# Kernel optimization log

Hardware: AMD Instinct MI355X
Metric: run time of the kernel (lower is better)

Reference implementation:

```python
import jax, jax.numpy as jnp
import numpy as np

D_IN = 1024
D_OUT = 1024
NUM_HEADS = 16
HEAD_DIM = D_OUT // NUM_HEADS


def setup_inputs() -> dict:
    key = jax.random.key(0)
    ks = jax.random.split(key, 6)
    s = 1.0 / np.sqrt(D_IN)
    x = jax.random.normal(ks[0], (2, 2048, D_IN), dtype=jnp.float32)
    Wq = jax.random.uniform(ks[1], (D_IN, D_OUT), jnp.float32, -s, s)
    Wk = jax.random.uniform(ks[2], (D_IN, D_OUT), jnp.float32, -s, s)
    Wv = jax.random.uniform(ks[3], (D_IN, D_OUT), jnp.float32, -s, s)
    Wo = jax.random.uniform(ks[4], (D_OUT, D_OUT), jnp.float32, -s, s)
    bo = jax.random.uniform(ks[5], (D_OUT,), jnp.float32, -s, s)
    return {"x": x, "Wq": Wq, "Wk": Wk, "Wv": Wv, "Wo": Wo, "bo": bo}


def reference(x, Wq, Wk, Wv, Wo, bo):
    b, s, _ = x.shape
    # Note: source assigns keys = W_query(x), queries = W_key(x) (swapped names);
    # replicate exactly.
    keys = (x @ Wq).reshape(b, s, NUM_HEADS, HEAD_DIM)
    values = (x @ Wv).reshape(b, s, NUM_HEADS, HEAD_DIM)
    queries = (x @ Wk).reshape(b, s, NUM_HEADS, HEAD_DIM)
    # [b, h, q, k] attention scores; source's masked_fill is non in-place and
    # discarded, so NO causal mask is applied (faithful to the bug).
    scores = jnp.einsum("bqhd,bkhd->bhqk", queries, keys)
    attn = jax.nn.softmax(scores / np.sqrt(HEAD_DIM), axis=-1)
    # dropout p=0.0 -> identity
    ctx = jnp.einsum("bhqk,bkhd->bqhd", attn, values).reshape(b, s, D_OUT)
    return ctx @ Wo + bo
```

## Files before the change

kernel.cpp:

```cpp
#include <hip/hip_runtime.h>
#include <math.h>

#define DI 1024
#define SQ 2048
#define NB 2
#define NH 16
#define HD 64
#define QSCALE 0.18033688f

typedef __attribute__((ext_vector_type(8))) short short8;
typedef __attribute__((ext_vector_type(4))) float f32x4;
typedef __attribute__((ext_vector_type(16))) float f32x16;
typedef __attribute__((ext_vector_type(2))) unsigned int uint2v;
typedef __attribute__((ext_vector_type(4))) int int4v;
typedef __attribute__((ext_vector_type(4))) unsigned short ushort4v;

static __device__ __forceinline__ unsigned short f2bf(float f) {
    union { float f; unsigned u; } v; v.f = f;
    unsigned r = v.u + 0x7FFFu + ((v.u >> 16) & 1u);
    return (unsigned short)(r >> 16);
}
static __device__ __forceinline__ float fexp2(float x) {
    float r; asm("v_exp_f32 %0, %1" : "=v"(r) : "v"(x)); return r;
}
static __device__ __forceinline__ unsigned cvtpk(float lo, float hi) {
    unsigned r; asm("v_cvt_pk_bf16_f32 %0, %1, %2" : "=v"(r) : "v"(lo), "v"(hi)); return r;
}
static __device__ __forceinline__ void plswap(unsigned& a, unsigned& b) {
    asm volatile("v_permlane32_swap_b32 %0, %1" : "+v"(a), "+v"(b));
}
static __device__ __forceinline__ short8 pack4(unsigned a, unsigned b, unsigned c, unsigned d) {
    union { unsigned u[4]; short8 s; } x; x.u[0] = a; x.u[1] = b; x.u[2] = c; x.u[3] = d; return x.s;
}

typedef __attribute__((address_space(1))) const unsigned int gas_uint;
typedef __attribute__((address_space(3))) unsigned int las_uint;
static __device__ __forceinline__ void gload16(const void* g, void* l) {
    __builtin_amdgcn_global_load_lds((gas_uint*)g, (las_uint*)l, 16, 0, 0);
}
#define RAW_BARRIER() __builtin_amdgcn_s_barrier()
#define WAIT_VM4()  do { asm volatile("s_waitcnt vmcnt(4)" ::: "memory"); \
                         __builtin_amdgcn_sched_barrier(0); } while (0)
#define WAIT_VM0()  do { asm volatile("s_waitcnt vmcnt(0)" ::: "memory"); \
                         __builtin_amdgcn_sched_barrier(0); } while (0)

#define MFMA16(a, b, c) __builtin_amdgcn_mfma_f32_16x16x32_bf16(a, b, c, 0, 0, 0)
#define MFMA32(a, b, c) __builtin_amdgcn_mfma_f32_32x32x16_bf16(a, b, c, 0, 0, 0)

__global__ __launch_bounds__(256) void k_cvt_bf16(const float* __restrict__ src,
                                                  unsigned short* __restrict__ dst) {
    int i = blockIdx.x * 256 + threadIdx.x;
    const f32x4* s4 = (const f32x4*)src + (size_t)i * 2;
    f32x4 a = s4[0], b = s4[1];
    ushort4v o0, o1;
    o0[0] = f2bf(a[0]); o0[1] = f2bf(a[1]); o0[2] = f2bf(a[2]); o0[3] = f2bf(a[3]);
    o1[0] = f2bf(b[0]); o1[1] = f2bf(b[1]); o1[2] = f2bf(b[2]); o1[3] = f2bf(b[3]);
    *(ushort4v*)(dst + (size_t)i * 8)     = o0;
    *(ushort4v*)(dst + (size_t)i * 8 + 4) = o1;
}

__global__ __launch_bounds__(256) void k_transpose_w4(const float* __restrict__ W0, const float* __restrict__ W1,
                                                      const float* __restrict__ W2, const float* __restrict__ W3,
                                                      unsigned short* __restrict__ T0, unsigned short* __restrict__ T1,
                                                      unsigned short* __restrict__ T2, unsigned short* __restrict__ T3) {
    const float* W; unsigned short* T;
    switch (blockIdx.z) {
        case 0: W = W0; T = T0; break;
        case 1: W = W1; T = T1; break;
        case 2: W = W2; T = T2; break;
        default: W = W3; T = T3; break;
    }
    __shared__ float t[32][33];
    int tx = threadIdx.x, ty = threadIdx.y;
    int n0 = blockIdx.x * 32, k0 = blockIdx.y * 32;
#pragma unroll
    for (int j = 0; j < 32; j += 8) t[ty + j][tx] = W[(size_t)(k0 + ty + j) * DI + n0 + tx];
    __syncthreads();
#pragma unroll
    for (int j = 0; j < 32; j += 8)
        T[(size_t)(n0 + ty + j) * DI + k0 + tx] = f2bf(t[tx][ty + j]);
}

template <int MODE>
__global__ __launch_bounds__(256) void k_gemm(const unsigned short* __restrict__ A,
                                              const unsigned short* __restrict__ Bt,
                                              unsigned short* __restrict__ oK,
                                              unsigned short* __restrict__ oQ,
                                              unsigned short* __restrict__ oV,
                                              const float* __restrict__ bias) {
    __shared__ __align__(16) unsigned short As[2][128 * 32];
    __shared__ __align__(16) unsigned short Bs[2][128 * 32];
    const int tid = threadIdx.x, lane = tid & 63, w = tid >> 6;
    const int wr = w >> 1, wc = w & 1;
    const int tm = blockIdx.y, tn = blockIdx.x;
    const unsigned short* Abase = A  + (size_t)tm * 128 * DI;
    const unsigned short* Bbase = Bt + (size_t)tn * 128 * DI;

    auto stage = [&](int kt, int bi) {
#pragma unroll
        for (int i = 0; i < 2; ++i) {
            int u = tid + i * 256;
            int row = u >> 2, c8 = (u & 3) * 8;
            gload16(Abase + (size_t)row * DI + kt * 32 + c8, &As[bi][u * 8]);
            gload16(Bbase + (size_t)row * DI + kt * 32 + c8, &Bs[bi][u * 8]);
        }
    };

    f32x4 acc[4][4] = {};
    stage(0, 0);
    for (int kt = 0; kt < DI / 32; ++kt) {
        RAW_BARRIER();
        if (kt + 1 < DI / 32) { stage(kt + 1, (kt + 1) & 1); WAIT_VM4(); }
        else                  { WAIT_VM0(); }
        const int bi = kt & 1;
        short8 af[4], bf[4];
#pragma unroll
        for (int mi = 0; mi < 4; ++mi)
            af[mi] = *(const short8*)&As[bi][(wr * 64 + mi * 16 + (lane & 15)) * 32 + (lane >> 4) * 8];
#pragma unroll
        for (int ni = 0; ni < 4; ++ni)
            bf[ni] = *(const short8*)&Bs[bi][(wc * 64 + ni * 16 + (lane & 15)) * 32 + (lane >> 4) * 8];
        __builtin_amdgcn_s_setprio(1);
#pragma unroll
        for (int mi = 0; mi < 4; ++mi)
#pragma unroll
            for (int ni = 0; ni < 4; ++ni)
                acc[mi][ni] = MFMA16(af[mi], bf[ni], acc[mi][ni]);
        __builtin_amdgcn_s_setprio(0);
    }

    if (MODE == 2) {
        float bv[4];
#pragma unroll
        for (int ni = 0; ni < 4; ++ni) bv[ni] = bias[tn * 128 + wc * 64 + ni * 16 + (lane & 15)];
        float* Co = (float*)oK;
#pragma unroll
        for (int mi = 0; mi < 4; ++mi)
#pragma unroll
            for (int ni = 0; ni < 4; ++ni)
#pragma unroll
                for (int j = 0; j < 4; ++j) {
                    int m = tm * 128 + wr * 64 + mi * 16 + (lane >> 4) * 4 + j;
                    int n = tn * 128 + wc * 64 + ni * 16 + (lane & 15);
                    Co[(size_t)m * DI + n] = acc[mi][ni][j] + bv[ni];
                }
    } else {
        const int which = tn >> 3;
        if (which < 2) {
            unsigned short* Co = which ? oQ : oK;
            const float scl = which ? QSCALE : 1.0f;
#pragma unroll
            for (int mi = 0; mi < 4; ++mi)
#pragma unroll
                for (int ni = 0; ni < 4; ++ni)
#pragma unroll
                    for (int j = 0; j < 4; ++j) {
                        int m = tm * 128 + wr * 64 + mi * 16 + (lane >> 4) * 4 + j;
                        int n = (tn & 7) * 128 + wc * 64 + ni * 16 + (lane & 15);
                        Co[(((size_t)(m >> 11) * NH + (n >> 6)) * SQ + (m & 2047)) * HD + (n & 63)] =
                            f2bf(acc[mi][ni][j] * scl);
                    }
        } else {
#pragma unroll
            for (int mi = 0; mi < 4; ++mi)
#pragma unroll
                for (int ni = 0; ni < 4; ++ni) {
                    uint2v pk;
                    pk[0] = cvtpk(acc[mi][ni][0], acc[mi][ni][1]);
                    pk[1] = cvtpk(acc[mi][ni][2], acc[mi][ni][3]);
                    int m = tm * 128 + wr * 64 + mi * 16 + (lane >> 4) * 4;
                    int n = (tn & 7) * 128 + wc * 64 + ni * 16 + (lane & 15);
                    *(uint2v*)&oV[(((size_t)(m >> 11) * NH + (n >> 6)) * HD + (n & 63)) * SQ + (m & 2047)] = pk;
                }
        }
    }
}

__global__ __launch_bounds__(256) void k_attn(const unsigned short* __restrict__ Q,
                                              const unsigned short* __restrict__ K,
                                              const unsigned short* __restrict__ Vt,
                                              unsigned short* __restrict__ ctx) {
    __shared__ __align__(16) unsigned short smem[16384];
    unsigned short* Ks = smem;
    unsigned short* Vs = smem + 8192;
    const int tid = threadIdx.x, lane = tid & 63, w = tid >> 6;
    const int hi = lane >> 5, l31 = lane & 31;

    const int wg = (blockIdx.x & 7) * 64 + (blockIdx.x >> 3);
    const int bh = wg >> 4;
    const int q0 = (wg & 15) * 128;

    const unsigned short* qh = Q  + (size_t)bh * SQ * HD;
    const unsigned short* kh = K  + (size_t)bh * SQ * HD;
    const unsigned short* vh = Vt + (size_t)bh * HD * SQ;

    short8 qf[4];
#pragma unroll
    for (int ks = 0; ks < 4; ++ks)
        qf[ks] = *(const short8*)(qh + (size_t)(q0 + w * 32 + l31) * HD + ks * 16 + hi * 8);

    short8 ones;
#pragma unroll
    for (int i = 0; i < 8; ++i) ones[i] = (short)0x3F80;

    f32x16 o[2] = {{0}, {0}};
    f32x16 od = {};

    auto stage = [&](int kt, int bi) {
#pragma unroll
        for (int i = 0; i < 2; ++i) {
            int u = tid + i * 256;
            int row = u >> 3, c = u & 7;
            int cs = c ^ (row & 7);
            gload16(kh + (size_t)(kt * 64 + row) * HD + cs * 8, Ks + bi * 4096 + u * 8);
            gload16(vh + (size_t)row * SQ + kt * 64 + cs * 8, Vs + bi * 4096 + u * 8);
        }
    };

    stage(0, 0);
    for (int kt = 0; kt < SQ / 64; ++kt) {
        RAW_BARRIER();
        if (kt + 1 < SQ / 64) { stage(kt + 1, (kt + 1) & 1); WAIT_VM4(); }
        else                  { WAIT_VM0(); }
        const unsigned short* kb_ = Ks + (kt & 1) * 4096;
        const unsigned short* vb_ = Vs + (kt & 1) * 4096;

#pragma unroll
        for (int kb = 0; kb < 2; ++kb) {
            f32x16 s = {};
            {
                short8 kf[4];
#pragma unroll
                for (int ks = 0; ks < 4; ++ks) {
                    int row = kb * 32 + l31;
                    kf[ks] = *(const short8*)&kb_[row * 64 + (((ks * 2 + hi) ^ (row & 7)) * 8)];
                }
                __builtin_amdgcn_s_setprio(1);
#pragma unroll
                for (int ks = 0; ks < 4; ++ks) s = MFMA32(kf[ks], qf[ks], s);
                __builtin_amdgcn_s_setprio(0);
            }

            float p[16];
#pragma unroll
            for (int r = 0; r < 16; ++r) p[r] = fexp2(s[r]);

            unsigned g0 = cvtpk(p[0],  p[1]),  g1 = cvtpk(p[2],  p[3]);
            unsigned g2 = cvtpk(p[4],  p[5]),  g3 = cvtpk(p[6],  p[7]);
            unsigned g4 = cvtpk(p[8],  p[9]),  g5 = cvtpk(p[10], p[11]);
            unsigned g6 = cvtpk(p[12], p[13]), g7 = cvtpk(p[14], p[15]);
            plswap(g0, g2); plswap(g1, g3);
            plswap(g4, g6); plswap(g5, g7);
            short8 pf[2] = { pack4(g0, g1, g2, g3), pack4(g4, g5, g6, g7) };

            short8 vf[2][2];
#pragma unroll
            for (int ks2 = 0; ks2 < 2; ++ks2)
#pragma unroll
                for (int da = 0; da < 2; ++da) {
                    int row = da * 32 + l31;
                    vf[ks2][da] = *(const short8*)&vb_[row * 64 + (((kb * 4 + ks2 * 2 + hi) ^ (row & 7)) * 8)];
                }
            __builtin_amdgcn_s_setprio(1);
#pragma unroll
            for (int ks2 = 0; ks2 < 2; ++ks2) {
#pragma unroll
                for (int da = 0; da < 2; ++da)
                    o[da] = MFMA32(vf[ks2][da], pf[ks2], o[da]);
                od = MFMA32(ones, pf[ks2], od);
            }
            __builtin_amdgcn_s_setprio(0);
        }
    }

    __syncthreads();

    float inv = 1.0f / od[0];

    unsigned short* osc = smem + w * 2304;
#pragma unroll
    for (int da = 0; da < 2; ++da)
#pragma unroll
        for (int g = 0; g < 4; ++g) {
            uint2v pk;
            pk[0] = cvtpk(o[da][4 * g]     * inv, o[da][4 * g + 1] * inv);
            pk[1] = cvtpk(o[da][4 * g + 2] * inv, o[da][4 * g + 3] * inv);
            int d = da * 32 + 8 * g + 4 * hi;
            *(uint2v*)&osc[l31 * 72 + d] = pk;
        }
    __syncthreads();

    const int b = bh >> 4, h = bh & 15;
#pragma unroll
    for (int rr = 0; rr < 4; ++rr) {
        int qrow = rr * 8 + (lane >> 3), ck = lane & 7;
        int4v vv = *(const int4v*)&osc[qrow * 72 + ck * 8];
        *(int4v*)&ctx[((size_t)(b * SQ + q0 + w * 32 + qrow)) * DI + h * 64 + ck * 8] = vv;
    }
}

extern "C" void kernel_launch(void* const* d_in, const int* in_sizes, int n_in,
                              void* d_out, int out_size, void* d_ws, size_t ws_size,
                              hipStream_t stream) {
    const float* x  = (const float*)d_in[0];
    const float* Wq = (const float*)d_in[1];
    const float* Wk = (const float*)d_in[2];
    const float* Wv = (const float*)d_in[3];
    const float* Wo = (const float*)d_in[4];
    const float* bo = (const float*)d_in[5];

    char* ws = (char*)d_ws;
    unsigned short* xb   = (unsigned short*)(ws);
    unsigned short* Wall = (unsigned short*)(ws + (8u  << 20));
    unsigned short* Wot  = (unsigned short*)(ws + (14u << 20));
    unsigned short* Qh   = (unsigned short*)(ws + (16u << 20));
    unsigned short* Kh   = (unsigned short*)(ws + (24u << 20));
    unsigned short* Vt   = (unsigned short*)(ws + (32u << 20));
    unsigned short* ctx  = (unsigned short*)(ws + (40u << 20));

    k_cvt_bf16<<<2048, 256, 0, stream>>>(x, xb);
    k_transpose_w4<<<dim3(32, 32, 4), dim3(32, 8), 0, stream>>>(
        Wq, Wk, Wv, Wo, Wall, Wall + (1u << 20), Wall + (2u << 20), Wot);

    k_gemm<0><<<dim3(24, 32), 256, 0, stream>>>(xb, Wall, Kh, Qh, Vt, nullptr);

    k_attn<<<dim3(512), 256, 0, stream>>>(Qh, Kh, Vt, ctx);

    k_gemm<2><<<dim3(8, 32), 256, 0, stream>>>(ctx, Wot, (unsigned short*)d_out, nullptr, nullptr, bo);
}
```

Measured before the change: 121.4 us.

## Triple-buffer LDS tiles and restructure attention loop for more MFMA overlap

Moves both the projection GEMM and the attention kernel from double to triple buffering in LDS. The next tile is issued and waited on before the barrier, so one barrier per iteration suffices. In the attention kernel, all K/V fragments for both 32-key sub-blocks are loaded up front, both score MFMAs run back to back, and two separate output accumulators are used and summed at the end. The goal is fewer stalls from MFMA dependency chains and from barriers, at the cost of more LDS and more registers, which may reduce occupancy.

```diff
diff --git a/kernel.cpp b/kernel.cpp
--- a/kernel.cpp
+++ b/kernel.cpp
@@ -38,7 +38,8 @@
 static __device__ __forceinline__ void gload16(const void* g, void* l) {
     __builtin_amdgcn_global_load_lds((gas_uint*)g, (las_uint*)l, 16, 0, 0);
 }
-#define RAW_BARRIER() __builtin_amdgcn_s_barrier()
+#define RAW_BARRIER() do { __builtin_amdgcn_s_barrier(); \
+                           __builtin_amdgcn_sched_barrier(0); } while (0)
 #define WAIT_VM4()  do { asm volatile("s_waitcnt vmcnt(4)" ::: "memory"); \
                          __builtin_amdgcn_sched_barrier(0); } while (0)
 #define WAIT_VM0()  do { asm volatile("s_waitcnt vmcnt(0)" ::: "memory"); \
@@ -88,8 +89,8 @@
                                               unsigned short* __restrict__ oQ,
                                               unsigned short* __restrict__ oV,
                                               const float* __restrict__ bias) {
-    __shared__ __align__(16) unsigned short As[2][128 * 32];
-    __shared__ __align__(16) unsigned short Bs[2][128 * 32];
+    __shared__ __align__(16) unsigned short As[3][128 * 32];
+    __shared__ __align__(16) unsigned short Bs[3][128 * 32];
     const int tid = threadIdx.x, lane = tid & 63, w = tid >> 6;
     const int wr = w >> 1, wc = w & 1;
     const int tm = blockIdx.y, tn = blockIdx.x;
@@ -109,10 +110,10 @@
     f32x4 acc[4][4] = {};
     stage(0, 0);
     for (int kt = 0; kt < DI / 32; ++kt) {
+        if (kt + 1 < DI / 32) { stage(kt + 1, (kt + 1) % 3); WAIT_VM4(); }
+        else                  { WAIT_VM0(); }
         RAW_BARRIER();
-        if (kt + 1 < DI / 32) { stage(kt + 1, (kt + 1) & 1); WAIT_VM4(); }
-        else                  { WAIT_VM0(); }
-        const int bi = kt & 1;
+        const int bi = kt % 3;
         short8 af[4], bf[4];
 #pragma unroll
         for (int mi = 0; mi < 4; ++mi)
@@ -180,9 +181,9 @@
                                               const unsigned short* __restrict__ K,
                                               const unsigned short* __restrict__ Vt,
                                               unsigned short* __restrict__ ctx) {
-    __shared__ __align__(16) unsigned short smem[16384];
+    __shared__ __align__(16) unsigned short smem[24576];
     unsigned short* Ks = smem;
-    unsigned short* Vs = smem + 8192;
+    unsigned short* Vs = smem + 12288;
     const int tid = threadIdx.x, lane = tid & 63, w = tid >> 6;
     const int hi = lane >> 5, l31 = lane & 31;
 
@@ -203,7 +204,8 @@
 #pragma unroll
     for (int i = 0; i < 8; ++i) ones[i] = (short)0x3F80;
 
-    f32x16 o[2] = {{0}, {0}};
+    f32x16 oA[2] = {{0}, {0}};
+    f32x16 oB[2] = {{0}, {0}};
     f32x16 od = {};
 
     auto stage = [&](int kt, int bi) {
@@ -219,58 +221,74 @@
 
     stage(0, 0);
     for (int kt = 0; kt < SQ / 64; ++kt) {
+        if (kt + 1 < SQ / 64) { stage(kt + 1, (kt + 1) % 3); WAIT_VM4(); }
+        else                  { WAIT_VM0(); }
         RAW_BARRIER();
-        if (kt + 1 < SQ / 64) { stage(kt + 1, (kt + 1) & 1); WAIT_VM4(); }
-        else                  { WAIT_VM0(); }
-        const unsigned short* kb_ = Ks + (kt & 1) * 4096;
-        const unsigned short* vb_ = Vs + (kt & 1) * 4096;
-
-#pragma unroll
-        for (int kb = 0; kb < 2; ++kb) {
-            f32x16 s = {};
-            {
-                short8 kf[4];
-#pragma unroll
-                for (int ks = 0; ks < 4; ++ks) {
-                    int row = kb * 32 + l31;
-                    kf[ks] = *(const short8*)&kb_[row * 64 + (((ks * 2 + hi) ^ (row & 7)) * 8)];
-                }
-                __builtin_amdgcn_s_setprio(1);
-#pragma unroll
-                for (int ks = 0; ks < 4; ++ks) s = MFMA32(kf[ks], qf[ks], s);
-                __builtin_amdgcn_s_setprio(0);
+        const unsigned short* kb_ = Ks + (kt % 3) * 4096;
+        const unsigned short* vb_ = Vs + (kt % 3) * 4096;
+
+        short8 kf[2][4], vf[2][2][2];
+#pragma unroll
+        for (int kb = 0; kb < 2; ++kb)
+#pragma unroll
+            for (int ks = 0; ks < 4; ++ks) {
+                int row = kb * 32 + l31;
+                kf[kb][ks] = *(const short8*)&kb_[row * 64 + (((ks * 2 + hi) ^ (row & 7)) * 8)];
             }
-
-            float p[16];
-#pragma unroll
-            for (int r = 0; r < 16; ++r) p[r] = fexp2(s[r]);
-
-            unsigned g0 = cvtpk(p[0],  p[1]),  g1 = cvtpk(p[2],  p[3]);
-            unsigned g2 = cvtpk(p[4],  p[5]),  g3 = cvtpk(p[6],  p[7]);
-            unsigned g4 = cvtpk(p[8],  p[9]),  g5 = cvtpk(p[10], p[11]);
-            unsigned g6 = cvtpk(p[12], p[13]), g7 = cvtpk(p[14], p[15]);
-            plswap(g0, g2); plswap(g1, g3);
-            plswap(g4, g6); plswap(g5, g7);
-            short8 pf[2] = { pack4(g0, g1, g2, g3), pack4(g4, g5, g6, g7) };
-
-            short8 vf[2][2];
+#pragma unroll
+        for (int kb = 0; kb < 2; ++kb)
 #pragma unroll
             for (int ks2 = 0; ks2 < 2; ++ks2)
 #pragma unroll
                 for (int da = 0; da < 2; ++da) {
                     int row = da * 32 + l31;
-                    vf[ks2][da] = *(const short8*)&vb_[row * 64 + (((kb * 4 + ks2 * 2 + hi) ^ (row & 7)) * 8)];
+                    vf[kb][ks2][da] = *(const short8*)&vb_[row * 64 + (((kb * 4 + ks2 * 2 + hi) ^ (row & 7)) * 8)];
                 }
-            __builtin_amdgcn_s_setprio(1);
-#pragma unroll
-            for (int ks2 = 0; ks2 < 2; ++ks2) {
-#pragma unroll
-                for (int da = 0; da < 2; ++da)
-                    o[da] = MFMA32(vf[ks2][da], pf[ks2], o[da]);
-                od = MFMA32(ones, pf[ks2], od);
-            }
-            __builtin_amdgcn_s_setprio(0);
-        }
+
+        f32x16 s0 = {}, s1 = {};
+        __builtin_amdgcn_s_setprio(1);
+#pragma unroll
+        for (int ks = 0; ks < 4; ++ks) s0 = MFMA32(kf[0][ks], qf[ks], s0);
+#pragma unroll
+        for (int ks = 0; ks < 4; ++ks) s1 = MFMA32(kf[1][ks], qf[ks], s1);
+        __builtin_amdgcn_s_setprio(0);
+
+        float p0[16], p1[16];
+#pragma unroll
+        for (int r = 0; r < 16; ++r) p0[r] = fexp2(s0[r]);
+#pragma unroll
+        for (int r = 0; r < 16; ++r) p1[r] = fexp2(s1[r]);
+
+        unsigned a0 = cvtpk(p0[0],  p0[1]),  a1 = cvtpk(p0[2],  p0[3]);
+        unsigned a2 = cvtpk(p0[4],  p0[5]),  a3 = cvtpk(p0[6],  p0[7]);
+        unsigned a4 = cvtpk(p0[8],  p0[9]),  a5 = cvtpk(p0[10], p0[11]);
+        unsigned a6 = cvtpk(p0[12], p0[13]), a7 = cvtpk(p0[14], p0[15]);
+        plswap(a0, a2); plswap(a1, a3); plswap(a4, a6); plswap(a5, a7);
+        short8 pf0[2] = { pack4(a0, a1, a2, a3), pack4(a4, a5, a6, a7) };
+
+        unsigned b0 = cvtpk(p1[0],  p1[1]),  b1 = cvtpk(p1[2],  p1[3]);
+        unsigned b2 = cvtpk(p1[4],  p1[5]),  b3 = cvtpk(p1[6],  p1[7]);
+        unsigned b4 = cvtpk(p1[8],  p1[9]),  b5 = cvtpk(p1[10], p1[11]);
+        unsigned b6 = cvtpk(p1[12], p1[13]), b7 = cvtpk(p1[14], p1[15]);
+        plswap(b0, b2); plswap(b1, b3); plswap(b4, b6); plswap(b5, b7);
+        short8 pf1[2] = { pack4(b0, b1, b2, b3), pack4(b4, b5, b6, b7) };
+
+        __builtin_amdgcn_s_setprio(1);
+#pragma unroll
+        for (int ks2 = 0; ks2 < 2; ++ks2) {
+#pragma unroll
+            for (int da = 0; da < 2; ++da)
+                oA[da] = MFMA32(vf[0][ks2][da], pf0[ks2], oA[da]);
+            od = MFMA32(ones, pf0[ks2], od);
+        }
+#pragma unroll
+        for (int ks2 = 0; ks2 < 2; ++ks2) {
+#pragma unroll
+            for (int da = 0; da < 2; ++da)
+                oB[da] = MFMA32(vf[1][ks2][da], pf1[ks2], oB[da]);
+            od = MFMA32(ones, pf1[ks2], od);
+        }
+        __builtin_amdgcn_s_setprio(0);
     }
 
     __syncthreads();
@@ -282,9 +300,12 @@
     for (int da = 0; da < 2; ++da)
 #pragma unroll
         for (int g = 0; g < 4; ++g) {
+            f32x16 om;
+#pragma unroll
+            for (int j = 0; j < 4; ++j) om[4 * g + j] = oA[da][4 * g + j] + oB[da][4 * g + j];
             uint2v pk;
-            pk[0] = cvtpk(o[da][4 * g]     * inv, o[da][4 * g + 1] * inv);
-            pk[1] = cvtpk(o[da][4 * g + 2] * inv, o[da][4 * g + 3] * inv);
+            pk[0] = cvtpk(om[4 * g]     * inv, om[4 * g + 1] * inv);
+            pk[1] = cvtpk(om[4 * g + 2] * inv, om[4 * g + 3] * inv);
             int d = da * 32 + 8 * g + 4 * hi;
             *(uint2v*)&osc[l31 * 72 + d] = pk;
         }
```

After: 123.0 us. No clear change (+1.4%).

## Split attention across key halves with combine pass; triple-buffer GEMM staging

Applied to the files above, without the earlier changes.

The attention kernel is split into two halves along the key dimension, launching 1024 workgroups instead of 512 so more CUs are occupied. Each half writes an unnormalized bf16 partial output and its denominator, and a new combine kernel sums the two partials and normalizes. The GEMM moves from double to triple buffering in LDS, with the barrier placed after the prefetch. The split adds an extra kernel plus extra global traffic and bf16 rounding of partials, and the attention loop now uses __syncthreads with no explicit vmcnt wait.

```diff
diff --git a/kernel.cpp b/kernel.cpp
--- a/kernel.cpp
+++ b/kernel.cpp
@@ -20,6 +20,9 @@
     unsigned r = v.u + 0x7FFFu + ((v.u >> 16) & 1u);
     return (unsigned short)(r >> 16);
 }
+static __device__ __forceinline__ float bf2f(unsigned short b) {
+    union { unsigned u; float f; } v; v.u = ((unsigned)b) << 16; return v.f;
+}
 static __device__ __forceinline__ float fexp2(float x) {
     float r; asm("v_exp_f32 %0, %1" : "=v"(r) : "v"(x)); return r;
 }
@@ -38,7 +41,8 @@
 static __device__ __forceinline__ void gload16(const void* g, void* l) {
     __builtin_amdgcn_global_load_lds((gas_uint*)g, (las_uint*)l, 16, 0, 0);
 }
-#define RAW_BARRIER() __builtin_amdgcn_s_barrier()
+#define RAW_BARRIER() do { __builtin_amdgcn_s_barrier(); \
+                           __builtin_amdgcn_sched_barrier(0); } while (0)
 #define WAIT_VM4()  do { asm volatile("s_waitcnt vmcnt(4)" ::: "memory"); \
                          __builtin_amdgcn_sched_barrier(0); } while (0)
 #define WAIT_VM0()  do { asm volatile("s_waitcnt vmcnt(0)" ::: "memory"); \
@@ -88,8 +92,8 @@
                                               unsigned short* __restrict__ oQ,
                                               unsigned short* __restrict__ oV,
                                               const float* __restrict__ bias) {
-    __shared__ __align__(16) unsigned short As[2][128 * 32];
-    __shared__ __align__(16) unsigned short Bs[2][128 * 32];
+    __shared__ __align__(16) unsigned short As[3][128 * 32];
+    __shared__ __align__(16) unsigned short Bs[3][128 * 32];
     const int tid = threadIdx.x, lane = tid & 63, w = tid >> 6;
     const int wr = w >> 1, wc = w & 1;
     const int tm = blockIdx.y, tn = blockIdx.x;
@@ -109,10 +113,10 @@
     f32x4 acc[4][4] = {};
     stage(0, 0);
     for (int kt = 0; kt < DI / 32; ++kt) {
+        if (kt + 1 < DI / 32) { stage(kt + 1, (kt + 1) % 3); WAIT_VM4(); }
+        else                  { WAIT_VM0(); }
         RAW_BARRIER();
-        if (kt + 1 < DI / 32) { stage(kt + 1, (kt + 1) & 1); WAIT_VM4(); }
-        else                  { WAIT_VM0(); }
-        const int bi = kt & 1;
+        const int bi = kt % 3;
         short8 af[4], bf[4];
 #pragma unroll
         for (int mi = 0; mi < 4; ++mi)
@@ -176,19 +180,25 @@
     }
 }
 
-__global__ __launch_bounds__(256) void k_attn(const unsigned short* __restrict__ Q,
-                                              const unsigned short* __restrict__ K,
-                                              const unsigned short* __restrict__ Vt,
-                                              unsigned short* __restrict__ ctx) {
+__global__ __launch_bounds__(256) void k_attn_part(const unsigned short* __restrict__ Q,
+                                                   const unsigned short* __restrict__ K,
+                                                   const unsigned short* __restrict__ Vt,
+                                                   unsigned short* __restrict__ PA,
+                                                   unsigned short* __restrict__ PB,
+                                                   float* __restrict__ dnA,
+                                                   float* __restrict__ dnB) {
     __shared__ __align__(16) unsigned short smem[16384];
     unsigned short* Ks = smem;
     unsigned short* Vs = smem + 8192;
     const int tid = threadIdx.x, lane = tid & 63, w = tid >> 6;
     const int hi = lane >> 5, l31 = lane & 31;
 
-    const int wg = (blockIdx.x & 7) * 64 + (blockIdx.x >> 3);
-    const int bh = wg >> 4;
-    const int q0 = (wg & 15) * 128;
+    const int wg = (blockIdx.x & 7) * 128 + (blockIdx.x >> 3);
+    const int bh = wg >> 5;
+    const int rest = wg & 31;
+    const int q0 = (rest >> 1) * 128;
+    const int half = rest & 1;
+    const int tbase = half * 16;
 
     const unsigned short* qh = Q  + (size_t)bh * SQ * HD;
     const unsigned short* kh = K  + (size_t)bh * SQ * HD;
@@ -206,24 +216,24 @@
     f32x16 o[2] = {{0}, {0}};
     f32x16 od = {};
 
-    auto stage = [&](int kt, int bi) {
+    auto stage = [&](int t, int bi) {
+        int gt = tbase + t;
 #pragma unroll
         for (int i = 0; i < 2; ++i) {
             int u = tid + i * 256;
             int row = u >> 3, c = u & 7;
             int cs = c ^ (row & 7);
-            gload16(kh + (size_t)(kt * 64 + row) * HD + cs * 8, Ks + bi * 4096 + u * 8);
-            gload16(vh + (size_t)row * SQ + kt * 64 + cs * 8, Vs + bi * 4096 + u * 8);
+            gload16(kh + (size_t)(gt * 64 + row) * HD + cs * 8, Ks + bi * 4096 + u * 8);
+            gload16(vh + (size_t)row * SQ + gt * 64 + cs * 8, Vs + bi * 4096 + u * 8);
         }
     };
 
     stage(0, 0);
-    for (int kt = 0; kt < SQ / 64; ++kt) {
-        RAW_BARRIER();
-        if (kt + 1 < SQ / 64) { stage(kt + 1, (kt + 1) & 1); WAIT_VM4(); }
-        else                  { WAIT_VM0(); }
-        const unsigned short* kb_ = Ks + (kt & 1) * 4096;
-        const unsigned short* vb_ = Vs + (kt & 1) * 4096;
+    for (int t = 0; t < 16; ++t) {
+        __syncthreads();
+        if (t + 1 < 16) stage(t + 1, (t + 1) & 1);
+        const unsigned short* kb_ = Ks + (t & 1) * 4096;
+        const unsigned short* vb_ = Vs + (t & 1) * 4096;
 
 #pragma unroll
         for (int kb = 0; kb < 2; ++kb) {
@@ -275,7 +285,8 @@
 
     __syncthreads();
 
-    float inv = 1.0f / od[0];
+    unsigned short* Pout = half ? PB : PA;
+    float*          dnO  = half ? dnB : dnA;
 
     unsigned short* osc = smem + w * 2304;
 #pragma unroll
@@ -283,8 +294,8 @@
 #pragma unroll
         for (int g = 0; g < 4; ++g) {
             uint2v pk;
-            pk[0] = cvtpk(o[da][4 * g]     * inv, o[da][4 * g + 1] * inv);
-            pk[1] = cvtpk(o[da][4 * g + 2] * inv, o[da][4 * g + 3] * inv);
+            pk[0] = cvtpk(o[da][4 * g],     o[da][4 * g + 1]);
+            pk[1] = cvtpk(o[da][4 * g + 2], o[da][4 * g + 3]);
             int d = da * 32 + 8 * g + 4 * hi;
             *(uint2v*)&osc[l31 * 72 + d] = pk;
         }
@@ -295,8 +306,32 @@
     for (int rr = 0; rr < 4; ++rr) {
         int qrow = rr * 8 + (lane >> 3), ck = lane & 7;
         int4v vv = *(const int4v*)&osc[qrow * 72 + ck * 8];
-        *(int4v*)&ctx[((size_t)(b * SQ + q0 + w * 32 + qrow)) * DI + h * 64 + ck * 8] = vv;
-    }
+        *(int4v*)&Pout[((size_t)(b * SQ + q0 + w * 32 + qrow)) * DI + h * 64 + ck * 8] = vv;
+    }
+    if (hi == 0)
+        dnO[(size_t)bh * SQ + q0 + w * 32 + l31] = od[0];
+}
+
+__global__ __launch_bounds__(256) void k_combine(unsigned short* __restrict__ PA,
+                                                 const unsigned short* __restrict__ PB,
+                                                 const float* __restrict__ dnA,
+                                                 const float* __restrict__ dnB) {
+    int i = blockIdx.x * 256 + threadIdx.x;
+    int m = i >> 7;
+    int ci = i & 127;
+    int q = m & (SQ - 1), b = m >> 11, h = ci >> 3;
+    size_t dn_i = (size_t)(b * NH + h) * SQ + q;
+    float inv = 1.0f / (dnA[dn_i] + dnB[dn_i]);
+    size_t off = (size_t)m * DI + ci * 8;
+    ushort4v a0 = *(const ushort4v*)(PA + off), a1 = *(const ushort4v*)(PA + off + 4);
+    ushort4v b0 = *(const ushort4v*)(PB + off), b1 = *(const ushort4v*)(PB + off + 4);
+    uint2v o0, o1;
+    o0[0] = cvtpk((bf2f(a0[0]) + bf2f(b0[0])) * inv, (bf2f(a0[1]) + bf2f(b0[1])) * inv);
+    o0[1] = cvtpk((bf2f(a0[2]) + bf2f(b0[2])) * inv, (bf2f(a0[3]) + bf2f(b0[3])) * inv);
+    o1[0] = cvtpk((bf2f(a1[0]) + bf2f(b1[0])) * inv, (bf2f(a1[1]) + bf2f(b1[1])) * inv);
+    o1[1] = cvtpk((bf2f(a1[2]) + bf2f(b1[2])) * inv, (bf2f(a1[3]) + bf2f(b1[3])) * inv);
+    *(uint2v*)(PA + off)     = o0;
+    *(uint2v*)(PA + off + 4) = o1;
 }
 
 extern "C" void kernel_launch(void* const* d_in, const int* in_sizes, int n_in,
@@ -318,13 +353,19 @@
     unsigned short* Vt   = (unsigned short*)(ws + (32u << 20));
     unsigned short* ctx  = (unsigned short*)(ws + (40u << 20));
 
+    unsigned short* PA  = ctx;
+    unsigned short* PB  = xb;
+    float*          dnA = (float*)(ws + (8u << 20));
+    float*          dnB = (float*)(ws + (9u << 20));
+
     k_cvt_bf16<<<2048, 256, 0, stream>>>(x, xb);
     k_transpose_w4<<<dim3(32, 32, 4), dim3(32, 8), 0, stream>>>(
         Wq, Wk, Wv, Wo, Wall, Wall + (1u << 20), Wall + (2u << 20), Wot);
 
     k_gemm<0><<<dim3(24, 32), 256, 0, stream>>>(xb, Wall, Kh, Qh, Vt, nullptr);
 
-    k_attn<<<dim3(512), 256, 0, stream>>>(Qh, Kh, Vt, ctx);
+    k_attn_part<<<dim3(1024), 256, 0, stream>>>(Qh, Kh, Vt, PA, PB, dnA, dnB);
+    k_combine<<<dim3(2048), 256, 0, stream>>>(PA, PB, dnA, dnB);
 
     k_gemm<2><<<dim3(8, 32), 256, 0, stream>>>(ctx, Wot, (unsigned short*)d_out, nullptr, nullptr, bo);
 }
```

New measurement: 124.6 us. 1.03x slower.
